# Kernel optimization log

Hardware: AMD Instinct MI355X
Metric: run time of the kernel (lower is better)

Reference implementation:

```python
import jax, jax.numpy as jnp
import numpy as np

N_EMBD = 1024
N_HEAD = 16

def setup_inputs() -> dict:
    key = jax.random.key(0)
    ks = jax.random.split(key, 5)
    s = 0.02
    return {
        "x": jax.random.normal(ks[0], (4, 2048, N_EMBD), dtype=jnp.float32),
        "w_attn": jax.random.normal(ks[1], (N_EMBD, 3 * N_EMBD), dtype=jnp.float32) * s,
        "b_attn": jnp.zeros((3 * N_EMBD,), dtype=jnp.float32),
        "w_proj": jax.random.normal(ks[2], (N_EMBD, N_EMBD), dtype=jnp.float32) * s,
        "b_proj": jnp.zeros((N_EMBD,), dtype=jnp.float32),
    }

def reference(x, w_attn, b_attn, w_proj, b_proj):
    B, T, C = x.shape
    H = N_HEAD
    D = C // H
    qkv = x @ w_attn + b_attn                       # [B,T,3C]
    q, k, v = jnp.split(qkv, 3, axis=-1)
    # [B,H,T,D]
    q = q.reshape(B, T, H, D).transpose(0, 2, 1, 3)
    k = k.reshape(B, T, H, D).transpose(0, 2, 1, 3)
    v = v.reshape(B, T, H, D).transpose(0, 2, 1, 3)
    scale = 1.0 / jnp.sqrt(jnp.asarray(D, dtype=x.dtype))
    attn = jnp.einsum("bhqd,bhkd->bhqk", q, k) * scale
    mask = jnp.tril(jnp.ones((T, T), dtype=bool))
    attn = jnp.where(mask, attn, jnp.asarray(-jnp.inf, dtype=attn.dtype))
    attn = jax.nn.softmax(attn, axis=-1)
    out = jnp.einsum("bhqk,bhkd->bhqd", attn, v)    # [B,H,T,D]
    out = out.transpose(0, 2, 1, 3).reshape(B, T, C)
    return out @ w_proj + b_proj
```

## Files before the change

kernel.cpp:

```cpp
#include <hip/hip_runtime.h>


typedef unsigned short u16b;
typedef __bf16 bf16x8 __attribute__((ext_vector_type(8)));
typedef float f32x4 __attribute__((ext_vector_type(4)));
typedef float f32x16 __attribute__((ext_vector_type(16)));
typedef unsigned short u16x4 __attribute__((ext_vector_type(4)));

#define AS1(p) ((const __attribute__((address_space(1))) void*)(p))
#define AS3(p) ((__attribute__((address_space(3))) void*)(p))
#define GLDS(g, l) __builtin_amdgcn_global_load_lds(AS1(g), AS3(l), 16, 0, 0)

__device__ __forceinline__ u16b bfr(float v) {
  union { float f; unsigned u; } x; x.f = v;
  unsigned r = x.u + 0x7fffu + ((x.u >> 16) & 1u);
  return (u16b)(r >> 16);
}

__device__ __forceinline__ unsigned pk2(float lo, float hi) {
  union { __bf16 h[2]; unsigned u; } t;
  t.h[0] = (__bf16)lo; t.h[1] = (__bf16)hi;
  return t.u;
}

__global__ __launch_bounds__(256) void cvt_bf16_kernel(
    const float* __restrict__ src, u16b* __restrict__ dst, int n4) {
  int i = blockIdx.x * 256 + threadIdx.x;
  const int stride = gridDim.x * 256;
  for (; i < n4; i += stride) {
    const float4 v = reinterpret_cast<const float4*>(src)[i];
    u16x4 o;
    o[0] = bfr(v.x); o[1] = bfr(v.y); o[2] = bfr(v.z); o[3] = bfr(v.w);
    reinterpret_cast<u16x4*>(dst)[i] = o;
  }
}

__global__ __launch_bounds__(256) void transpose_cvt_kernel(
    const float* __restrict__ src, u16b* __restrict__ dst, int R, int C) {
  __shared__ u16b tile[64][72];
  const int nc = C >> 6;
  const int br = blockIdx.x / nc, bc = blockIdx.x % nc;
  const int r0 = br << 6, c0 = bc << 6;
  const int c = threadIdx.x & 63, r4 = threadIdx.x >> 6;
  #pragma unroll
  for (int i = 0; i < 16; ++i) {
    const int r = r4 + 4 * i;
    tile[r][c] = bfr(src[(size_t)(r0 + r) * C + c0 + c]);
  }
  __syncthreads();
  #pragma unroll
  for (int i = 0; i < 16; ++i) {
    const int rr = r4 + 4 * i;
    dst[(size_t)(c0 + rr) * R + r0 + c] = tile[c][rr];
  }
}

template <int EPI>
__global__ __launch_bounds__(256, 2) void gemm128_kernel(
    const u16b* __restrict__ A, const u16b* __restrict__ Bt,
    const float* __restrict__ bias,
    u16b* __restrict__ oQ, u16b* __restrict__ oK, u16b* __restrict__ oVt,
    float* __restrict__ oF, int M, int N, int K) {
  __shared__ u16b smem[32768];
  const int tid = threadIdx.x;
  const int wid = tid >> 6, lane = tid & 63;
  const int xcd = blockIdx.x & 7;
  const int idx = blockIdx.x >> 3;
  const int stg = idx >> 6, rr6 = idx & 63;
  const int brow = (xcd << 3) + (rr6 >> 3);
  const int bcol = (stg << 3) + (rr6 & 7);
  const int wr = (wid >> 1) << 6, wc = (wid & 1) << 6;

  f32x4 acc[4][4] = {};

  const int srow = (wid << 5) + (lane >> 3);
  const int sc = ((lane & 7) ^ (lane >> 3)) << 3;
  const u16b* Ab = A + (size_t)((brow << 7) + srow) * K + sc;
  const u16b* Bb = Bt + (size_t)((bcol << 7) + srow) * K + sc;
  const int fr = lane & 15;
  const int fq = lane >> 4;
  const int pcs0 = ((fq) ^ (fr & 7)) << 4;
  const int pcs1 = ((4 + fq) ^ (fr & 7)) << 4;
  const int nk = K >> 6;

#define STAGE(bufi, kk)                                                        \
  {                                                                            \
    char* sb = (char*)smem + (bufi) * 32768;                                   \
    _Pragma("unroll")                                                          \
    for (int j = 0; j < 4; ++j)                                                \
      GLDS(Ab + (size_t)8 * K * j + (kk), sb + wid * 4096 + j * 1024);         \
    _Pragma("unroll")                                                          \
    for (int j = 0; j < 4; ++j)                                                \
      GLDS(Bb + (size_t)8 * K * j + (kk), sb + 16384 + wid * 4096 + j * 1024); \
  }

  STAGE(0, 0);
  STAGE(1, 64);

  #pragma unroll 1
  for (int kt = 0; kt < nk; ++kt) {
    if (kt + 1 < nk) asm volatile("s_waitcnt vmcnt(8)" ::: "memory");
    else             asm volatile("s_waitcnt vmcnt(0)" ::: "memory");
    __builtin_amdgcn_s_barrier();

    const char* As = (const char*)smem + (kt & 1) * 32768;
    const char* Bs = As + 16384;
    bf16x8 af0[4], af1[4], bf0[4], bf1[4];
    #pragma unroll
    for (int i = 0; i < 4; ++i) {
      const int rowb = (wr + i * 16 + fr) * 128;
      af0[i] = *(const bf16x8*)(As + rowb + pcs0);
      af1[i] = *(const bf16x8*)(As + rowb + pcs1);
    }
    #pragma unroll
    for (int j = 0; j < 4; ++j) {
      const int rowb = (wc + j * 16 + fr) * 128;
      bf0[j] = *(const bf16x8*)(Bs + rowb + pcs0);
      bf1[j] = *(const bf16x8*)(Bs + rowb + pcs1);
    }
    __builtin_amdgcn_s_setprio(1);
    #pragma unroll
    for (int i = 0; i < 4; ++i)
      #pragma unroll
      for (int j = 0; j < 4; ++j)
        acc[i][j] = __builtin_amdgcn_mfma_f32_16x16x32_bf16(af0[i], bf0[j], acc[i][j], 0, 0, 0);
    #pragma unroll
    for (int i = 0; i < 4; ++i)
      #pragma unroll
      for (int j = 0; j < 4; ++j)
        acc[i][j] = __builtin_amdgcn_mfma_f32_16x16x32_bf16(af1[i], bf1[j], acc[i][j], 0, 0, 0);
    __builtin_amdgcn_s_setprio(0);

    __builtin_amdgcn_s_barrier();
    if (kt + 2 < nk) STAGE(kt & 1, (kt + 2) << 6);
  }
#undef STAGE

  if (EPI == 1) {
    #pragma unroll
    for (int j = 0; j < 4; ++j) {
      const int n0 = (bcol << 7) + wc + j * 16 + fr;
      const float bv = bias[n0];
      #pragma unroll
      for (int i = 0; i < 4; ++i) {
        #pragma unroll
        for (int r = 0; r < 4; ++r) {
          const int m0 = (brow << 7) + wr + i * 16 + fq * 4 + r;
          oF[(size_t)m0 * N + n0] = acc[i][j][r] + bv;
        }
      }
    }
  } else {
    const int sect = bcol >> 3;
    if (sect < 2) {
      const float qs = (sect == 0) ? 0.1803368801f : 1.0f;
      u16b* oPtr = (sect == 0) ? oQ : oK;
      u16b* tile = (u16b*)smem;
      #pragma unroll
      for (int j = 0; j < 4; ++j) {
        const int n = wc + j * 16 + fr;
        const float bv = bias[(bcol << 7) + n];
        #pragma unroll
        for (int i = 0; i < 4; ++i) {
          #pragma unroll
          for (int r = 0; r < 4; ++r) {
            const int m = wr + i * 16 + fq * 4 + r;
            const int byteoff = m * 256 + (((n >> 3) ^ (m & 7)) << 4) + ((n & 7) << 1);
            *(u16b*)((char*)tile + byteoff) = bfr((acc[i][j][r] + bv) * qs);
          }
        }
      }
      __syncthreads();
      const int nh = wid >> 1;
      const int c = lane & 7;
      #pragma unroll
      for (int it = 0; it < 8; ++it) {
        const int m = ((wid & 1) << 6) + (it << 3) + (lane >> 3);
        const int chunk = (nh << 3) + (c ^ (m & 7));
        const bf16x8 val = *(const bf16x8*)((const char*)tile + m * 256 + chunk * 16);
        const int m0 = (brow << 7) + m;
        const int n0 = (bcol << 7) + (nh << 6) + (c << 3);
        const int bb = m0 >> 11, tt = m0 & 2047;
        const int h = (n0 >> 6) & 15, d = n0 & 63;
        *(bf16x8*)(oPtr + (((size_t)(bb * 16 + h) * 2048 + tt) * 64 + d)) = val;
      }
    } else {
      u16b* tile = (u16b*)smem;
      #pragma unroll
      for (int j = 0; j < 4; ++j) {
        const int nl = wc + j * 16 + fr;
        const float bv = bias[(bcol << 7) + nl];
        #pragma unroll
        for (int i = 0; i < 4; ++i) {
          #pragma unroll
          for (int r = 0; r < 4; ++r) {
            const int m = wr + i * 16 + fq * 4 + r;
            const int byteoff = nl * 256 + (((m >> 3) ^ (nl & 7)) << 4) + ((m & 7) << 1);
            *(u16b*)((char*)tile + byteoff) = bfr(acc[i][j][r] + bv);
          }
        }
      }
      __syncthreads();
      const int row0 = wid << 5;
      const int c16 = lane & 15;
      const int rw = lane >> 4;
      const int t0 = (brow << 7) & 2047;
      const int bb = brow >> 4;
      #pragma unroll
      for (int it = 0; it < 8; ++it) {
        const int nl = row0 + (it << 2) + rw;
        const int pch = c16 ^ (nl & 7);
        const bf16x8 val = *(const bf16x8*)((const char*)tile + nl * 256 + pch * 16);
        const int h = ((bcol & 7) << 1) + (nl >> 6);
        const int d = nl & 63;
        *(bf16x8*)(oVt + ((size_t)((bb << 4) + h) * 64 + d) * 2048 + t0 + (c16 << 3)) = val;
      }
    }
  }
}

__global__ __launch_bounds__(256, 4) void flash_kernel(
    const u16b* __restrict__ Q, const u16b* __restrict__ K,
    const u16b* __restrict__ Vt, u16b* __restrict__ O) {
  __shared__ u16b smem[16384];
  const int bid = blockIdx.x;
  const int bh = bid & 63;
  const int slot = bid >> 6;
  const int sg = slot & 3, sp = slot >> 2;
  const int qt = (sp & 1) ? (2 * sg + (sp >> 1)) : (15 - (sp >> 1) - 2 * sg);
  const int tid = threadIdx.x, wid = tid >> 6, lane = tid & 63;
  const int ln31 = lane & 31, hi = lane >> 5;
  const size_t baseQK = (size_t)bh * 2048 * 64;
  const size_t baseV = (size_t)bh * 64 * 2048;
  const int b = bh >> 4, h = bh & 15;
  const int srow = wid * 8 + (lane >> 3);
  const int sc = ((lane & 7) ^ (srow & 7)) << 3;

  const int q0w = (qt << 7) + wid * 32;
  const int NT = 2 * qt + 2;
  const int LT = q0w >> 6;

#define FSTAGE(kt, bi)                                                         \
  {                                                                            \
    char* kb_ = (char*)smem + (bi) * 16384;                                    \
    const int k0_ = (kt) << 6;                                                 \
    GLDS(K + baseQK + (size_t)(k0_ + srow) * 64 + sc,        kb_ + wid * 1024);\
    GLDS(K + baseQK + (size_t)(k0_ + 32 + srow) * 64 + sc,   kb_ + 4096 + wid * 1024);\
    GLDS(Vt + baseV + (size_t)srow * 2048 + k0_ + sc,        kb_ + 8192 + wid * 1024);\
    GLDS(Vt + baseV + (size_t)(32 + srow) * 2048 + k0_ + sc, kb_ + 12288 + wid * 1024);\
  }

  bf16x8 qf[4];
  {
    const u16b* qp = Q + baseQK + (size_t)(q0w + ln31) * 64 + hi * 8;
    #pragma unroll
    for (int kk = 0; kk < 4; ++kk) qf[kk] = *(const bf16x8*)(qp + kk * 16);
  }
  bf16x8 ones;
  {
    union { u16b s[8]; bf16x8 v; } o1;
    #pragma unroll
    for (int i = 0; i < 8; ++i) o1.s[i] = 0x3F80;
    ones = o1.v;
  }

  f32x16 oa0 = {}, oa1 = {}, lacc = {};

  FSTAGE(0, 0);
  FSTAGE(1, 1);

  #pragma unroll 1
  for (int kt = 0; kt < NT; ++kt) {
    if (kt + 1 < NT) asm volatile("s_waitcnt vmcnt(4)" ::: "memory");
    else             asm volatile("s_waitcnt vmcnt(0)" ::: "memory");
    __builtin_amdgcn_s_barrier();

    if (kt <= LT) {
      const char* kb = (const char*)smem + (kt & 1) * 16384;
      const char* vb = kb + 8192;
      const bool diag = (kt == LT);
      const int maxsub = diag ? (wid & 1) : 1;

      f32x16 s[2] = {};
      __builtin_amdgcn_s_setprio(1);
      #pragma unroll
      for (int ss = 0; ss < 2; ++ss) {
        if (ss <= maxsub) {
          const int row = 32 * ss + ln31;
          #pragma unroll
          for (int kk = 0; kk < 4; ++kk) {
            const int ch = (2 * kk + hi) ^ (row & 7);
            const bf16x8 kf = *(const bf16x8*)(kb + row * 128 + ch * 16);
            s[ss] = __builtin_amdgcn_mfma_f32_32x32x16_bf16(kf, qf[kk], s[ss], 0, 0, 0);
          }
        }
      }
      __builtin_amdgcn_s_setprio(0);

      if (diag) {
        #pragma unroll
        for (int ss = 0; ss < 2; ++ss) {
          if (ss == (wid & 1)) {
            #pragma unroll
            for (int r = 0; r < 16; ++r) {
              const int kvr = (r & 3) + 8 * (r >> 2) + 4 * hi;
              if (kvr > ln31) s[ss][r] = -3e38f;
            }
          }
        }
      }

      #pragma unroll
      for (int ss = 0; ss < 2; ++ss) {
        if (ss <= maxsub) {
          #pragma unroll
          for (int r = 0; r < 16; ++r)
            s[ss][r] = __builtin_amdgcn_exp2f(s[ss][r]);
        }
      }

      union WB { unsigned u[4]; bf16x8 v; };
      __builtin_amdgcn_s_setprio(1);
      #pragma unroll
      for (int ss = 0; ss < 2; ++ss) {
        if (ss <= maxsub) {
          WB pA, pB;
#define MKPA(W0, W1, W2, W3, P0, P1, P2, P3, P4, P5, P6, P7)                 \
          {                                                                   \
            unsigned a0 = pk2(P0, P1), a1 = pk2(P2, P3);                      \
            unsigned b0 = pk2(P4, P5), b1 = pk2(P6, P7);                      \
            auto r0 = __builtin_amdgcn_permlane32_swap(a0, b0, false, false); \
            auto r1 = __builtin_amdgcn_permlane32_swap(a1, b1, false, false); \
            unsigned o0[2], o1[2];                                            \
            __builtin_memcpy(o0, &r0, 8); __builtin_memcpy(o1, &r1, 8);       \
            W0 = o0[0]; W2 = o0[1]; W1 = o1[0]; W3 = o1[1];                   \
          }
          MKPA(pA.u[0], pA.u[1], pA.u[2], pA.u[3],
               s[ss][0], s[ss][1], s[ss][2], s[ss][3],
               s[ss][4], s[ss][5], s[ss][6], s[ss][7]);
          MKPA(pB.u[0], pB.u[1], pB.u[2], pB.u[3],
               s[ss][8], s[ss][9], s[ss][10], s[ss][11],
               s[ss][12], s[ss][13], s[ss][14], s[ss][15]);
#undef MKPA
          const int r0v = ln31, r1v = 32 + ln31;
          const char* v0 = vb + r0v * 128;
          const char* v1 = vb + r1v * 128;
          const int chA0 = ((4 * ss + hi) ^ (r0v & 7)) << 4;
          const int chA1 = ((4 * ss + hi) ^ (r1v & 7)) << 4;
          const int chB0 = ((4 * ss + 2 + hi) ^ (r0v & 7)) << 4;
          const int chB1 = ((4 * ss + 2 + hi) ^ (r1v & 7)) << 4;
          lacc = __builtin_amdgcn_mfma_f32_32x32x16_bf16(ones, pA.v, lacc, 0, 0, 0);
          oa0 = __builtin_amdgcn_mfma_f32_32x32x16_bf16(*(const bf16x8*)(v0 + chA0), pA.v, oa0, 0, 0, 0);
          oa1 = __builtin_amdgcn_mfma_f32_32x32x16_bf16(*(const bf16x8*)(v1 + chA1), pA.v, oa1, 0, 0, 0);
          lacc = __builtin_amdgcn_mfma_f32_32x32x16_bf16(ones, pB.v, lacc, 0, 0, 0);
          oa0 = __builtin_amdgcn_mfma_f32_32x32x16_bf16(*(const bf16x8*)(v0 + chB0), pB.v, oa0, 0, 0, 0);
          oa1 = __builtin_amdgcn_mfma_f32_32x32x16_bf16(*(const bf16x8*)(v1 + chB1), pB.v, oa1, 0, 0, 0);
        }
      }
      __builtin_amdgcn_s_setprio(0);
    }

    __builtin_amdgcn_s_barrier();
    if (kt + 2 < NT) FSTAGE(kt + 2, kt & 1);
  }

  const float inv = 1.0f / lacc[0];
  const int q = q0w + ln31;
  u16b* orow = O + (size_t)(b * 2048 + q) * 1024 + h * 64;
  #pragma unroll
  for (int rq = 0; rq < 4; ++rq) {
    u16x4 v0, v1;
    #pragma unroll
    for (int j = 0; j < 4; ++j) {
      v0[j] = bfr(oa0[4 * rq + j] * inv);
      v1[j] = bfr(oa1[4 * rq + j] * inv);
    }
    const int d0 = 8 * rq + 4 * hi;
    *(u16x4*)(orow + d0) = v0;
    *(u16x4*)(orow + 32 + d0) = v1;
  }
#undef FSTAGE
}

extern "C" void kernel_launch(void* const* d_in, const int* in_sizes, int n_in,
                              void* d_out, int out_size, void* d_ws, size_t ws_size,
                              hipStream_t stream) {
  const float* x      = (const float*)d_in[0];
  const float* w_attn = (const float*)d_in[1];
  const float* b_attn = (const float*)d_in[2];
  const float* w_proj = (const float*)d_in[3];
  const float* b_proj = (const float*)d_in[4];
  float* out = (float*)d_out;
  char* ws = (char*)d_ws;

  u16b* xb  = (u16b*)(ws + 0);
  u16b* waT = (u16b*)(ws + 16777216);
  u16b* wpT = (u16b*)(ws + 23068672);
  u16b* Qb  = (u16b*)(ws + 25165824);
  u16b* Kb  = (u16b*)(ws + 41943040);
  u16b* Vtb = (u16b*)(ws + 75497472);
  u16b* attn = xb;

  cvt_bf16_kernel<<<2048, 256, 0, stream>>>(x, xb, (8192 * 1024) / 4);
  transpose_cvt_kernel<<<16 * 48, 256, 0, stream>>>(w_attn, waT, 1024, 3072);
  transpose_cvt_kernel<<<16 * 16, 256, 0, stream>>>(w_proj, wpT, 1024, 1024);
  gemm128_kernel<0><<<64 * 24, 256, 0, stream>>>(xb, waT, b_attn, Qb, Kb, Vtb, nullptr,
                                                 8192, 3072, 1024);
  flash_kernel<<<1024, 256, 0, stream>>>(Qb, Kb, Vtb, attn);
  gemm128_kernel<1><<<64 * 8, 256, 0, stream>>>(attn, wpT, b_proj, nullptr, nullptr, nullptr,
                                                out, 8192, 1024, 1024);
}
```

Baseline: 161.8 us.

## Split long causal query tiles across two KV halves and merge partials

Query tiles 8–15, which carry the most causal KV work, are each split into two blocks that cover separate halves of the key range. Each half writes unnormalized bf16 partial outputs plus row sums to workspace. A new merge kernel adds the two halves and normalizes them into the attention buffer. The grid grows from 1024 to 1536 blocks so work is spread more evenly across CUs. The cost is an extra kernel launch, extra global traffic for the partials, and some precision loss from storing unnormalized partials in bf16.

```diff
diff --git a/kernel.cpp b/kernel.cpp
--- a/kernel.cpp
+++ b/kernel.cpp
@@ -221,13 +221,19 @@
 
 __global__ __launch_bounds__(256, 4) void flash_kernel(
     const u16b* __restrict__ Q, const u16b* __restrict__ K,
-    const u16b* __restrict__ Vt, u16b* __restrict__ O) {
+    const u16b* __restrict__ Vt, u16b* __restrict__ O,
+    u16b* __restrict__ psum, float* __restrict__ lsum) {
   __shared__ u16b smem[16384];
   const int bid = blockIdx.x;
   const int bh = bid & 63;
   const int slot = bid >> 6;
-  const int sg = slot & 3, sp = slot >> 2;
-  const int qt = (sp & 1) ? (2 * sg + (sp >> 1)) : (15 - (sp >> 1) - 2 * sg);
+  const int m3 = slot % 3, d3 = slot / 3;
+  int qt, half, split;
+  if (m3 < 2) { const int hI = d3 * 2 + m3; qt = 15 - (hI >> 1); half = hI & 1; split = 1; }
+  else        { qt = 7 - d3; half = 0; split = 0; }
+  const int ktBeg = split ? half * (qt + 1) : 0;
+  const int ktEnd = split ? (ktBeg + qt + 1) : (2 * qt + 2);
+
   const int tid = threadIdx.x, wid = tid >> 6, lane = tid & 63;
   const int ln31 = lane & 31, hi = lane >> 5;
   const size_t baseQK = (size_t)bh * 2048 * 64;
@@ -237,7 +243,6 @@
   const int sc = ((lane & 7) ^ (srow & 7)) << 3;
 
   const int q0w = (qt << 7) + wid * 32;
-  const int NT = 2 * qt + 2;
   const int LT = q0w >> 6;
 
 #define FSTAGE(kt, bi)                                                         \
@@ -266,13 +271,13 @@
 
   f32x16 oa0 = {}, oa1 = {}, lacc = {};
 
-  FSTAGE(0, 0);
-  FSTAGE(1, 1);
+  FSTAGE(ktBeg, ktBeg & 1);
+  FSTAGE(ktBeg + 1, (ktBeg + 1) & 1);
 
   #pragma unroll 1
-  for (int kt = 0; kt < NT; ++kt) {
-    if (kt + 1 < NT) asm volatile("s_waitcnt vmcnt(4)" ::: "memory");
-    else             asm volatile("s_waitcnt vmcnt(0)" ::: "memory");
+  for (int kt = ktBeg; kt < ktEnd; ++kt) {
+    if (kt + 1 < ktEnd) asm volatile("s_waitcnt vmcnt(4)" ::: "memory");
+    else                asm volatile("s_waitcnt vmcnt(0)" ::: "memory");
     __builtin_amdgcn_s_barrier();
 
     if (kt <= LT) {
@@ -361,25 +366,72 @@
     }
 
     __builtin_amdgcn_s_barrier();
-    if (kt + 2 < NT) FSTAGE(kt + 2, kt & 1);
-  }
-
-  const float inv = 1.0f / lacc[0];
-  const int q = q0w + ln31;
-  u16b* orow = O + (size_t)(b * 2048 + q) * 1024 + h * 64;
+    if (kt + 2 < ktEnd) FSTAGE(kt + 2, kt & 1);
+  }
+
+  if (split) {
+    const int seg = (qt - 8) * 2 + half;
+    const int row = wid * 32 + ln31;
+    u16b* prow = psum + (((size_t)seg * 64 + bh) * 128 + row) * 64;
+    #pragma unroll
+    for (int rq = 0; rq < 4; ++rq) {
+      u16x4 v0, v1;
+      #pragma unroll
+      for (int j = 0; j < 4; ++j) {
+        v0[j] = bfr(oa0[4 * rq + j]);
+        v1[j] = bfr(oa1[4 * rq + j]);
+      }
+      const int d0 = 8 * rq + 4 * hi;
+      *(u16x4*)(prow + d0) = v0;
+      *(u16x4*)(prow + 32 + d0) = v1;
+    }
+    if (hi == 0) lsum[seg * 8192 + bh * 128 + row] = lacc[0];
+  } else {
+    const float inv = 1.0f / lacc[0];
+    const int q = q0w + ln31;
+    u16b* orow = O + (size_t)(b * 2048 + q) * 1024 + h * 64;
+    #pragma unroll
+    for (int rq = 0; rq < 4; ++rq) {
+      u16x4 v0, v1;
+      #pragma unroll
+      for (int j = 0; j < 4; ++j) {
+        v0[j] = bfr(oa0[4 * rq + j] * inv);
+        v1[j] = bfr(oa1[4 * rq + j] * inv);
+      }
+      const int d0 = 8 * rq + 4 * hi;
+      *(u16x4*)(orow + d0) = v0;
+      *(u16x4*)(orow + 32 + d0) = v1;
+    }
+  }
+#undef FSTAGE
+}
+
+__global__ __launch_bounds__(256) void merge_kernel(
+    const u16b* __restrict__ psum, const float* __restrict__ lsum,
+    u16b* __restrict__ attn) {
+  const int c = blockIdx.x * 256 + threadIdx.x;
+  const int dc = c & 7;
+  const int row = (c >> 3) & 127;
+  const int bh = (c >> 10) & 63;
+  const int g = c >> 16;
+  const size_t o0 = (((size_t)(g * 2) * 64 + bh) * 128 + row) * 64 + dc * 8;
+  const size_t o1 = (((size_t)(g * 2 + 1) * 64 + bh) * 128 + row) * 64 + dc * 8;
+  const bf16x8 a = *(const bf16x8*)(psum + o0);
+  const bf16x8 bb = *(const bf16x8*)(psum + o1);
+  const float l = lsum[(g * 2) * 8192 + bh * 128 + row] +
+                  lsum[(g * 2 + 1) * 8192 + bh * 128 + row];
+  const float inv = 1.0f / l;
+  u16x4 v0, v1;
   #pragma unroll
-  for (int rq = 0; rq < 4; ++rq) {
-    u16x4 v0, v1;
-    #pragma unroll
-    for (int j = 0; j < 4; ++j) {
-      v0[j] = bfr(oa0[4 * rq + j] * inv);
-      v1[j] = bfr(oa1[4 * rq + j] * inv);
-    }
-    const int d0 = 8 * rq + 4 * hi;
-    *(u16x4*)(orow + d0) = v0;
-    *(u16x4*)(orow + 32 + d0) = v1;
-  }
-#undef FSTAGE
+  for (int j = 0; j < 4; ++j) {
+    v0[j] = bfr(((float)a[j] + (float)bb[j]) * inv);
+    v1[j] = bfr(((float)a[j + 4] + (float)bb[j + 4]) * inv);
+  }
+  const int q = (g + 8) * 128 + row;
+  const int b = bh >> 4, hh = bh & 15;
+  u16b* dst = attn + (size_t)(b * 2048 + q) * 1024 + hh * 64 + dc * 8;
+  *(u16x4*)(dst) = v0;
+  *(u16x4*)(dst + 4) = v1;
 }
 
 extern "C" void kernel_launch(void* const* d_in, const int* in_sizes, int n_in,
@@ -393,12 +445,14 @@
   float* out = (float*)d_out;
   char* ws = (char*)d_ws;
 
-  u16b* xb  = (u16b*)(ws + 0);
-  u16b* waT = (u16b*)(ws + 16777216);
-  u16b* wpT = (u16b*)(ws + 23068672);
-  u16b* Qb  = (u16b*)(ws + 25165824);
-  u16b* Kb  = (u16b*)(ws + 41943040);
-  u16b* Vtb = (u16b*)(ws + 75497472);
+  u16b* xb   = (u16b*)(ws + 0);
+  u16b* waT  = (u16b*)(ws + 16777216);
+  u16b* wpT  = (u16b*)(ws + 23068672);
+  u16b* Qb   = (u16b*)(ws + 25165824);
+  u16b* Kb   = (u16b*)(ws + 41943040);
+  u16b* psum = (u16b*)(ws + 58720256);
+  u16b* Vtb  = (u16b*)(ws + 75497472);
+  float* lsum = (float*)(ws + 16777216);
   u16b* attn = xb;
 
   cvt_bf16_kernel<<<2048, 256, 0, stream>>>(x, xb, (8192 * 1024) / 4);
@@ -406,7 +460,8 @@
   transpose_cvt_kernel<<<16 * 16, 256, 0, stream>>>(w_proj, wpT, 1024, 1024);
   gemm128_kernel<0><<<64 * 24, 256, 0, stream>>>(xb, waT, b_attn, Qb, Kb, Vtb, nullptr,
                                                  8192, 3072, 1024);
-  flash_kernel<<<1024, 256, 0, stream>>>(Qb, Kb, Vtb, attn);
+  flash_kernel<<<1536, 256, 0, stream>>>(Qb, Kb, Vtb, attn, psum, lsum);
+  merge_kernel<<<2048, 256, 0, stream>>>(psum, lsum, attn);
   gemm128_kernel<1><<<64 * 8, 256, 0, stream>>>(attn, wpT, b_proj, nullptr, nullptr, nullptr,
                                                 out, 8192, 1024, 1024);
 }
```

New measurement: 170.9 us. 5.6% more time.

## Switch GEMMs to 256x128 tiles with 512-thread blocks and BK=32

Applied to the files above, without the earlier changes.

Both projection GEMMs now use 256x128 output tiles computed by 8 waves (512 threads) with a 32-wide K step, in place of 128x128 tiles with 4 waves and a 64-wide K step. Each wave still owns a 64x64 sub-tile, but the block shares a larger A tile, which cuts global and LDS traffic per output. The grid swizzle, LDS swizzles and epilogue write-out are reworked for the larger tile. In exchange there are twice as many K iterations, each with barriers, a smaller per-stage prefetch, and fewer blocks in flight (768 and 256), which may underfill the GPU on the output projection.

```diff
diff --git a/kernel.cpp b/kernel.cpp
--- a/kernel.cpp
+++ b/kernel.cpp
@@ -56,7 +56,7 @@
 }
 
 template <int EPI>
-__global__ __launch_bounds__(256, 2) void gemm128_kernel(
+__global__ __launch_bounds__(512, 4) void gemm256_kernel(
     const u16b* __restrict__ A, const u16b* __restrict__ Bt,
     const float* __restrict__ bias,
     u16b* __restrict__ oQ, u16b* __restrict__ oK, u16b* __restrict__ oVt,
@@ -64,89 +64,74 @@
   __shared__ u16b smem[32768];
   const int tid = threadIdx.x;
   const int wid = tid >> 6, lane = tid & 63;
+  const int wm = wid >> 1, wn = wid & 1;
   const int xcd = blockIdx.x & 7;
   const int idx = blockIdx.x >> 3;
-  const int stg = idx >> 6, rr6 = idx & 63;
-  const int brow = (xcd << 3) + (rr6 >> 3);
-  const int bcol = (stg << 3) + (rr6 & 7);
-  const int wr = (wid >> 1) << 6, wc = (wid & 1) << 6;
+  const int bcg = idx >> 4, r16 = idx & 15;
+  const int brow = (xcd << 2) + (r16 >> 2);
+  const int bcol = (bcg << 2) + (r16 & 3);
 
   f32x4 acc[4][4] = {};
 
-  const int srow = (wid << 5) + (lane >> 3);
-  const int sc = ((lane & 7) ^ (lane >> 3)) << 3;
-  const u16b* Ab = A + (size_t)((brow << 7) + srow) * K + sc;
-  const u16b* Bb = Bt + (size_t)((bcol << 7) + srow) * K + sc;
+  const int sr = lane >> 2;
+  const int scol = (((lane & 3) ^ (sr & 3))) << 3;
+  const u16b* Ab = A + (size_t)((brow << 8) + (wid << 5) + sr) * K + scol;
+  const u16b* Bb = Bt + (size_t)((bcol << 7) + (wid << 4) + sr) * K + scol;
   const int fr = lane & 15;
   const int fq = lane >> 4;
-  const int pcs0 = ((fq) ^ (fr & 7)) << 4;
-  const int pcs1 = ((4 + fq) ^ (fr & 7)) << 4;
-  const int nk = K >> 6;
-
-#define STAGE(bufi, kk)                                                        \
+  const int pcs = ((fq ^ (fr & 3))) << 4;
+  const int nk = K >> 5;
+
+#define STAGE(t)                                                               \
   {                                                                            \
-    char* sb = (char*)smem + (bufi) * 32768;                                   \
-    _Pragma("unroll")                                                          \
-    for (int j = 0; j < 4; ++j)                                                \
-      GLDS(Ab + (size_t)8 * K * j + (kk), sb + wid * 4096 + j * 1024);         \
-    _Pragma("unroll")                                                          \
-    for (int j = 0; j < 4; ++j)                                                \
-      GLDS(Bb + (size_t)8 * K * j + (kk), sb + 16384 + wid * 4096 + j * 1024); \
-  }
-
-  STAGE(0, 0);
-  STAGE(1, 64);
+    char* sb = (char*)smem + ((t) & 1) * 24576;                                \
+    GLDS(Ab + (size_t)(t) * 32,          sb + (wid * 2) * 1024);               \
+    GLDS(Ab + (size_t)16 * K + (size_t)(t) * 32, sb + (wid * 2 + 1) * 1024);   \
+    GLDS(Bb + (size_t)(t) * 32,          sb + 16384 + wid * 1024);             \
+  }
+
+  STAGE(0);
+  STAGE(1);
 
   #pragma unroll 1
   for (int kt = 0; kt < nk; ++kt) {
-    if (kt + 1 < nk) asm volatile("s_waitcnt vmcnt(8)" ::: "memory");
+    if (kt < nk - 1) asm volatile("s_waitcnt vmcnt(3)" ::: "memory");
     else             asm volatile("s_waitcnt vmcnt(0)" ::: "memory");
     __builtin_amdgcn_s_barrier();
 
-    const char* As = (const char*)smem + (kt & 1) * 32768;
+    const char* As = (const char*)smem + (kt & 1) * 24576;
     const char* Bs = As + 16384;
-    bf16x8 af0[4], af1[4], bf0[4], bf1[4];
-    #pragma unroll
-    for (int i = 0; i < 4; ++i) {
-      const int rowb = (wr + i * 16 + fr) * 128;
-      af0[i] = *(const bf16x8*)(As + rowb + pcs0);
-      af1[i] = *(const bf16x8*)(As + rowb + pcs1);
-    }
+    bf16x8 af[4], bfv[4];
+    #pragma unroll
+    for (int i = 0; i < 4; ++i)
+      af[i] = *(const bf16x8*)(As + ((wm << 6) + i * 16 + fr) * 64 + pcs);
+    #pragma unroll
+    for (int j = 0; j < 4; ++j)
+      bfv[j] = *(const bf16x8*)(Bs + ((wn << 6) + j * 16 + fr) * 64 + pcs);
+    __builtin_amdgcn_s_setprio(1);
+    #pragma unroll
+    for (int i = 0; i < 4; ++i)
+      #pragma unroll
+      for (int j = 0; j < 4; ++j)
+        acc[i][j] = __builtin_amdgcn_mfma_f32_16x16x32_bf16(af[i], bfv[j], acc[i][j], 0, 0, 0);
+    __builtin_amdgcn_s_setprio(0);
+
+    __builtin_amdgcn_s_barrier();
+    if (kt + 2 < nk) STAGE(kt + 2);
+  }
+#undef STAGE
+
+  if (EPI == 1) {
     #pragma unroll
     for (int j = 0; j < 4; ++j) {
-      const int rowb = (wc + j * 16 + fr) * 128;
-      bf0[j] = *(const bf16x8*)(Bs + rowb + pcs0);
-      bf1[j] = *(const bf16x8*)(Bs + rowb + pcs1);
-    }
-    __builtin_amdgcn_s_setprio(1);
-    #pragma unroll
-    for (int i = 0; i < 4; ++i)
-      #pragma unroll
-      for (int j = 0; j < 4; ++j)
-        acc[i][j] = __builtin_amdgcn_mfma_f32_16x16x32_bf16(af0[i], bf0[j], acc[i][j], 0, 0, 0);
-    #pragma unroll
-    for (int i = 0; i < 4; ++i)
-      #pragma unroll
-      for (int j = 0; j < 4; ++j)
-        acc[i][j] = __builtin_amdgcn_mfma_f32_16x16x32_bf16(af1[i], bf1[j], acc[i][j], 0, 0, 0);
-    __builtin_amdgcn_s_setprio(0);
-
-    __builtin_amdgcn_s_barrier();
-    if (kt + 2 < nk) STAGE(kt & 1, (kt + 2) << 6);
-  }
-#undef STAGE
-
-  if (EPI == 1) {
-    #pragma unroll
-    for (int j = 0; j < 4; ++j) {
-      const int n0 = (bcol << 7) + wc + j * 16 + fr;
+      const int n0 = (bcol << 7) + (wn << 6) + j * 16 + fr;
       const float bv = bias[n0];
       #pragma unroll
       for (int i = 0; i < 4; ++i) {
         #pragma unroll
-        for (int r = 0; r < 4; ++r) {
-          const int m0 = (brow << 7) + wr + i * 16 + fq * 4 + r;
-          oF[(size_t)m0 * N + n0] = acc[i][j][r] + bv;
+        for (int rr = 0; rr < 4; ++rr) {
+          const int m0 = (brow << 8) + (wm << 6) + i * 16 + fq * 4 + rr;
+          oF[(size_t)m0 * N + n0] = acc[i][j][rr] + bv;
         }
       }
     }
@@ -155,65 +140,60 @@
     if (sect < 2) {
       const float qs = (sect == 0) ? 0.1803368801f : 1.0f;
       u16b* oPtr = (sect == 0) ? oQ : oK;
-      u16b* tile = (u16b*)smem;
+      char* tile = (char*)smem;
       #pragma unroll
       for (int j = 0; j < 4; ++j) {
-        const int n = wc + j * 16 + fr;
+        const int n = (wn << 6) + j * 16 + fr;
         const float bv = bias[(bcol << 7) + n];
         #pragma unroll
         for (int i = 0; i < 4; ++i) {
           #pragma unroll
-          for (int r = 0; r < 4; ++r) {
-            const int m = wr + i * 16 + fq * 4 + r;
-            const int byteoff = m * 256 + (((n >> 3) ^ (m & 7)) << 4) + ((n & 7) << 1);
-            *(u16b*)((char*)tile + byteoff) = bfr((acc[i][j][r] + bv) * qs);
+          for (int rr = 0; rr < 4; ++rr) {
+            const int m = (wm << 6) + i * 16 + fq * 4 + rr;
+            const int byteoff = m * 256 + (((n >> 3) ^ (m & 15)) << 4) + ((n & 7) << 1);
+            *(u16b*)(tile + byteoff) = bfr((acc[i][j][rr] + bv) * qs);
           }
         }
       }
       __syncthreads();
-      const int nh = wid >> 1;
-      const int c = lane & 7;
-      #pragma unroll
-      for (int it = 0; it < 8; ++it) {
-        const int m = ((wid & 1) << 6) + (it << 3) + (lane >> 3);
-        const int chunk = (nh << 3) + (c ^ (m & 7));
-        const bf16x8 val = *(const bf16x8*)((const char*)tile + m * 256 + chunk * 16);
-        const int m0 = (brow << 7) + m;
-        const int n0 = (bcol << 7) + (nh << 6) + (c << 3);
-        const int bb = m0 >> 11, tt = m0 & 2047;
-        const int h = (n0 >> 6) & 15, d = n0 & 63;
+      const int c8 = tid & 15;
+      #pragma unroll
+      for (int rd = 0; rd < 8; ++rd) {
+        const int m = rd * 32 + (tid >> 4);
+        const bf16x8 val = *(const bf16x8*)(tile + m * 256 + ((c8 ^ (m & 15)) << 4));
+        const int m0 = (brow << 8) + m;
+        const int tt = m0 & 2047, bb = m0 >> 11;
+        const int h = ((bcol & 7) << 1) + (c8 >> 3);
+        const int d = (c8 & 7) << 3;
         *(bf16x8*)(oPtr + (((size_t)(bb * 16 + h) * 2048 + tt) * 64 + d)) = val;
       }
     } else {
-      u16b* tile = (u16b*)smem;
+      char* tile = (char*)smem;
       #pragma unroll
       for (int j = 0; j < 4; ++j) {
-        const int nl = wc + j * 16 + fr;
-        const float bv = bias[(bcol << 7) + nl];
+        const int n = (wn << 6) + j * 16 + fr;
+        const float bv = bias[(bcol << 7) + n];
         #pragma unroll
         for (int i = 0; i < 4; ++i) {
           #pragma unroll
-          for (int r = 0; r < 4; ++r) {
-            const int m = wr + i * 16 + fq * 4 + r;
-            const int byteoff = nl * 256 + (((m >> 3) ^ (nl & 7)) << 4) + ((m & 7) << 1);
-            *(u16b*)((char*)tile + byteoff) = bfr(acc[i][j][r] + bv);
+          for (int rr = 0; rr < 4; ++rr) {
+            const int m = (wm << 6) + i * 16 + fq * 4 + rr;
+            const int byteoff = n * 512 + (((m >> 3) ^ (n & 31)) << 4) + ((m & 7) << 1);
+            *(u16b*)(tile + byteoff) = bfr(acc[i][j][rr] + bv);
           }
         }
       }
       __syncthreads();
-      const int row0 = wid << 5;
-      const int c16 = lane & 15;
-      const int rw = lane >> 4;
-      const int t0 = (brow << 7) & 2047;
-      const int bb = brow >> 4;
-      #pragma unroll
-      for (int it = 0; it < 8; ++it) {
-        const int nl = row0 + (it << 2) + rw;
-        const int pch = c16 ^ (nl & 7);
-        const bf16x8 val = *(const bf16x8*)((const char*)tile + nl * 256 + pch * 16);
-        const int h = ((bcol & 7) << 1) + (nl >> 6);
-        const int d = nl & 63;
-        *(bf16x8*)(oVt + ((size_t)((bb << 4) + h) * 64 + d) * 2048 + t0 + (c16 << 3)) = val;
+      const int mc = tid & 31;
+      const int t0 = (brow & 7) << 8;
+      const int bb = brow >> 3;
+      #pragma unroll
+      for (int rd = 0; rd < 8; ++rd) {
+        const int n = rd * 16 + (tid >> 5);
+        const bf16x8 val = *(const bf16x8*)(tile + n * 512 + ((mc ^ (n & 31)) << 4));
+        const int h = ((bcol & 7) << 1) + (n >> 6);
+        const int d = n & 63;
+        *(bf16x8*)(oVt + ((size_t)((bb << 4) + h) * 64 + d) * 2048 + t0 + (mc << 3)) = val;
       }
     }
   }
@@ -404,9 +384,9 @@
   cvt_bf16_kernel<<<2048, 256, 0, stream>>>(x, xb, (8192 * 1024) / 4);
   transpose_cvt_kernel<<<16 * 48, 256, 0, stream>>>(w_attn, waT, 1024, 3072);
   transpose_cvt_kernel<<<16 * 16, 256, 0, stream>>>(w_proj, wpT, 1024, 1024);
-  gemm128_kernel<0><<<64 * 24, 256, 0, stream>>>(xb, waT, b_attn, Qb, Kb, Vtb, nullptr,
-                                                 8192, 3072, 1024);
+  gemm256_kernel<0><<<768, 512, 0, stream>>>(xb, waT, b_attn, Qb, Kb, Vtb, nullptr,
+                                             8192, 3072, 1024);
   flash_kernel<<<1024, 256, 0, stream>>>(Qb, Kb, Vtb, attn);
-  gemm128_kernel<1><<<64 * 8, 256, 0, stream>>>(attn, wpT, b_proj, nullptr, nullptr, nullptr,
-                                                out, 8192, 1024, 1024);
-}
+  gemm256_kernel<1><<<256, 512, 0, stream>>>(attn, wpT, b_proj, nullptr, nullptr, nullptr,
+                                             out, 8192, 1024, 1024);
+}
```

Result: slower. 167.0 us (+3.2%).
